# Kernel optimization log

Hardware: AMD Instinct MI355X
Metric: run time of the kernel (lower is better)

## Reference

```python
import jax, jax.numpy as jnp
import numpy as np

D_MODEL = 1024
H = 16           # num_heads
D = 64           # head_dim
HD = H * D       # hd_dim
PHASE_SCALE = 10.0


def _freqs():
    # Multiscale phasor frequencies (H, D): rotary-style per-dim decay,
    # per-head linear scale (reconstruction of generate_multiscale_phasors).
    d = jnp.arange(D, dtype=jnp.float32)
    base = 10000.0 ** (-d / D)                                  # (D,)
    head_scale = (jnp.arange(H, dtype=jnp.float32) + 1.0) / H   # (H,)
    return 2.0 * np.pi * head_scale[:, None] * base[None, :]    # (H, D)


def setup_inputs() -> dict:
    key = jax.random.key(0)
    ks = jax.random.split(key, 4)
    B, T = 2, 8192
    s = 1.0 / np.sqrt(D_MODEL)
    return {
        "x": jax.random.normal(ks[0], (B, T, D_MODEL), jnp.float32),
        "Wk": jax.random.normal(ks[1], (HD, D_MODEL), jnp.float32) * s,
        "Wv": jax.random.normal(ks[2], (HD, D_MODEL), jnp.float32) * s,
        "Wo": jax.random.normal(ks[3], (D_MODEL, HD), jnp.float32) * s,
        "gate": jnp.ones((H, 2), jnp.float32) * 0.5,
    }


def reference(x, Wk, Wv, Wo, gate):
    B, T, C = x.shape
    k_real = (x @ Wk.T).reshape(B, T, H, D)                      # (B,T,H,D)
    v = (x @ Wv.T).reshape(B, T, H, D).astype(jnp.complex64)
    # shared q/k unit-modulus phasors
    k = jnp.exp(1j * (k_real * PHASE_SCALE))                     # complex64
    q = k
    t = jnp.arange(T, dtype=jnp.float32)
    rotors = jnp.exp(1j * (t[:, None, None] * _freqs()[None]))   # (T,H,D)
    scale = jnp.sqrt(jnp.arange(1, T + 1, dtype=jnp.float32))[None, :, None, None]
    # positional path: bind with rotors, accumulate, retrieve with conj rotors
    mem_pos = jnp.cumsum(v * rotors[None], axis=1)
    out_pos = (mem_pos * jnp.conj(rotors)[None]).real / scale
    # associative path: bind with conj of shifted keys, retrieve with q
    k_shifted = jnp.roll(k, shift=1, axis=1).at[:, 0].set(0)
    mem_assoc = jnp.cumsum(v * jnp.conj(k_shifted), axis=1)
    out_assoc = (mem_assoc * q).real / scale
    # gated combine per head
    out = out_pos * gate[None, None, :, 0:1] + out_assoc * gate[None, None, :, 1:2]
    out = out.reshape(B, T, HD)
    return out @ Wo.T
```

## Files before the change

### kernel.cpp

```cpp
#include <hip/hip_runtime.h>
#include <math.h>


#define B_SZ 2
#define T_LEN 8192
#define H_N 16
#define D_N 64
#define HD 1024
#define DM 1024

#define NCH 128
#define CH (T_LEN / NCH)

typedef unsigned short u16;
typedef __attribute__((ext_vector_type(4))) unsigned short u16x4;
typedef __attribute__((ext_vector_type(8))) short s16x8;
typedef __attribute__((ext_vector_type(8))) _Float16 f16x8;
typedef __attribute__((ext_vector_type(4))) float f32x4;

__device__ __forceinline__ u16 f2h(float f) {
    return __builtin_bit_cast(u16, (_Float16)f);
}
__device__ __forceinline__ float h2f(u16 h) {
    return (float)__builtin_bit_cast(_Float16, h);
}

__global__ __launch_bounds__(256) void conv_x_h(
    const float* __restrict__ x, u16* __restrict__ xh)
{
    size_t i = ((size_t)blockIdx.x * 256 + threadIdx.x) * 4;
    float4 v = *reinterpret_cast<const float4*>(&x[i]);
    u16x4 o = { f2h(v.x), f2h(v.y), f2h(v.z), f2h(v.w) };
    *reinterpret_cast<u16x4*>(&xh[i]) = o;
}

__global__ __launch_bounds__(256) void conv_weights(
    const float* __restrict__ Wk, const float* __restrict__ Wv,
    const float* __restrict__ Wo, u16* __restrict__ Wkv, u16* __restrict__ Wob)
{
    size_t i = ((size_t)blockIdx.x * 256 + threadIdx.x) * 4;
    int r = (int)(i >> 10);
    size_t src = i & (1024ull * 1024 - 1);
    float4 v;
    float s = 1.f;
    u16* dst;
    size_t doff;
    if (r < 1024)      { v = *reinterpret_cast<const float4*>(&Wk[src]); s = 10.f; dst = Wkv; doff = i; }
    else if (r < 2048) { v = *reinterpret_cast<const float4*>(&Wv[src]); dst = Wkv; doff = i; }
    else               { v = *reinterpret_cast<const float4*>(&Wo[src]); dst = Wob; doff = src; }
    u16x4 o = { f2h(s * v.x), f2h(s * v.y), f2h(s * v.z), f2h(s * v.w) };
    *reinterpret_cast<u16x4*>(&dst[doff]) = o;
}

#define GBK 64

#define BAR()     asm volatile("s_barrier" ::: "memory")
#define VMCNT4()  asm volatile("s_waitcnt vmcnt(4)" ::: "memory")
#define VMCNT0()  asm volatile("s_waitcnt vmcnt(0)" ::: "memory")
#define LGKM8PRE() asm volatile("s_waitcnt lgkmcnt(8)" ::: "memory")
#define LGKM0_SB() do { asm volatile("s_waitcnt lgkmcnt(0)" ::: "memory"); \
                        __builtin_amdgcn_sched_barrier(0); } while (0)

template <int IMM>
__device__ __forceinline__ s16x8 dsr(unsigned base) {
    s16x8 r;
    asm volatile("ds_read_b128 %0, %1 offset:%2"
                 : "=v"(r) : "v"(base), "n"(IMM));
    return r;
}

__device__ __forceinline__ unsigned lds_addr(const void* p) {
    return (unsigned)(uintptr_t)(const __attribute__((address_space(3))) void*)p;
}

#define MFMA_Q(mh, nh)                                               \
  {                                                                  \
    _Pragma("unroll")                                                \
    for (int ks_ = 0; ks_ < 2; ++ks_)                                \
      _Pragma("unroll")                                              \
      for (int m_ = 0; m_ < 4; ++m_)                                 \
        _Pragma("unroll")                                            \
        for (int n_ = 0; n_ < 2; ++n_)                               \
          acc[(mh)*4 + m_][(nh)*2 + n_] =                            \
            __builtin_amdgcn_mfma_f32_16x16x32_f16(                  \
              __builtin_bit_cast(f16x8, aR[m_][ks_]),                \
              __builtin_bit_cast(f16x8, bR[(nh)*2 + n_][ks_]),       \
              acc[(mh)*4 + m_][(nh)*2 + n_], 0, 0, 0);               \
  }

#define RD_A(ph, ofs)                                                          \
  aR[0][0]=dsr<(ofs)+0>(bA[ph][0]);    aR[1][0]=dsr<(ofs)+2048>(bA[ph][0]);    \
  aR[2][0]=dsr<(ofs)+4096>(bA[ph][0]); aR[3][0]=dsr<(ofs)+6144>(bA[ph][0]);    \
  aR[0][1]=dsr<(ofs)+0>(bA[ph][1]);    aR[1][1]=dsr<(ofs)+2048>(bA[ph][1]);    \
  aR[2][1]=dsr<(ofs)+4096>(bA[ph][1]); aR[3][1]=dsr<(ofs)+6144>(bA[ph][1]);
#define RD_B01(ph)                                                             \
  bR[0][0]=dsr<0>(bB[ph][0]);    bR[1][0]=dsr<2048>(bB[ph][0]);                \
  bR[0][1]=dsr<0>(bB[ph][1]);    bR[1][1]=dsr<2048>(bB[ph][1]);
#define RD_B23(ph)                                                             \
  bR[2][0]=dsr<4096>(bB[ph][0]); bR[3][0]=dsr<6144>(bB[ph][0]);                \
  bR[2][1]=dsr<4096>(bB[ph][1]); bR[3][1]=dsr<6144>(bB[ph][1]);

#define PHASE_GROUP(ph)                                              \
  {                                                                  \
    RD_A(ph, 0); RD_B01(ph); RD_B23(ph);                             \
    LGKM8PRE();                                                      \
    if ((ph) == 0)    { STAGE_A(2*t+1, 1, 0); STAGE_A(2*t+1, 1, 1); }\
    else if (gm)      { STAGE_A(2*t+2, 0, 0); STAGE_A(2*t+2, 0, 1); }\
    BAR(); LGKM0_SB();                                               \
    __builtin_amdgcn_s_setprio(1);                                   \
    MFMA_Q(0, 0); MFMA_Q(0, 1);                                      \
    __builtin_amdgcn_s_setprio(0);                                   \
    BAR();                                                           \
    RD_A(ph, 8192);                                                  \
    if (gm) { STAGE_B(2*t+2+(ph), (ph), 0);                          \
              STAGE_B(2*t+2+(ph), (ph), 1); VMCNT4(); }              \
    else    { VMCNT0(); }                                            \
    BAR(); LGKM0_SB();                                               \
    __builtin_amdgcn_s_setprio(1);                                   \
    MFMA_Q(1, 0); MFMA_Q(1, 1);                                      \
    __builtin_amdgcn_s_setprio(0);                                   \
    BAR();                                                           \
  }

__device__ __forceinline__ void stage_half(
    const u16* __restrict__ g, int ld, int rowbase, int kbase,
    char* ldshalf, int wid, int lane)
{
#pragma unroll
    for (int s = 0; s < 2; ++s) {
        const int slot = s * 512 + wid * 64 + lane;
        const int r = slot >> 3;
        const int cb = ((slot & 7) << 4) ^ ((r & 7) << 4);
        const u16* gp = g + (size_t)(rowbase + r) * ld + kbase + (cb >> 1);
        __builtin_amdgcn_global_load_lds(
            (const __attribute__((address_space(1))) void*)gp,
            (__attribute__((address_space(3))) void*)(ldshalf + s * 8192 + wid * 1024),
            16, 0, 0);
    }
}

__global__ __launch_bounds__(512, 2) void gemm_mfma256(
    const u16* __restrict__ A, int lda, const u16* __restrict__ W, int ldw,
    void* __restrict__ Cv, int ldc, void* __restrict__ Vv, int K, int mode,
    int m_base, int bshift)
{
    __shared__ __align__(16) char lds[131072];

    const int tid  = threadIdx.x;
    const int lane = tid & 63;
    const int wid  = tid >> 6;
    const int wm   = wid >> 2;
    const int wn   = wid & 3;
    const int l15  = lane & 15;
    const int hib  = (lane >> 4) << 4;

    const int flat = blockIdx.y * gridDim.x + blockIdx.x;
    const int xcd  = flat & 7;
    const int c    = flat >> 3;
    const int byl  = c & ((1 << bshift) - 1);
    const int bx   = c >> bshift;
    const int m0   = ((xcd << bshift) + byl) * 256 + m_base;
    const int n0   = bx * 256;

    const int NK2 = K / (2 * GBK);

    f32x4 acc[8][4] = {};
    s16x8 aR[4][2], bR[4][2];

    const int Xl = (l15 & 7) << 4;
    unsigned bA[2][2], bB[2][2];
#pragma unroll
    for (int p2 = 0; p2 < 2; ++p2)
#pragma unroll
        for (int ks = 0; ks < 2; ++ks) {
            bA[p2][ks] = lds_addr(lds) + p2 * 65536 +
                         (wm * 128 + l15) * 128 + ((ks * 64 + hib) ^ Xl);
            bB[p2][ks] = lds_addr(lds) + p2 * 65536 + 32768 +
                         (wn * 64 + l15) * 128 + ((ks * 64 + hib) ^ Xl);
        }

    auto STAGE_A = [&](int kt, int buf, int h) {
        stage_half(A, lda, m0 + h * 128, kt * GBK,
                   (char*)lds + buf * 65536 + h * 16384, wid, lane);
    };
    auto STAGE_B = [&](int kt, int buf, int h) {
        stage_half(W, ldw, n0 + h * 128, kt * GBK,
                   (char*)lds + buf * 65536 + 32768 + h * 16384, wid, lane);
    };

    STAGE_B(0, 0, 0); STAGE_B(0, 0, 1);
    STAGE_A(0, 0, 0); STAGE_A(0, 0, 1);
    STAGE_B(1, 1, 0); STAGE_B(1, 1, 1);
    VMCNT4();
    BAR();

    for (int t = 0; t < NK2; ++t) {
        const bool gm = (t < NK2 - 1);
        PHASE_GROUP(0)
        PHASE_GROUP(1)
    }

    const float TWOPI  = 6.2831853071795864f;
    const float INV2PI = 0.15915494309189535f;
    float* Cf = (float*)Cv;
    u16*   Ph = (u16*)Cv;
    u16*   Vh = (u16*)Vv;
    const bool isPhase = (n0 < 1024);
#pragma unroll
    for (int m = 0; m < 8; ++m) {
#pragma unroll
        for (int n = 0; n < 4; ++n) {
            const int r0  = m0 + wm * 128 + m * 16 + ((lane >> 4) << 2);
            const int col = n0 + wn * 64 + n * 16 + l15;
#pragma unroll
            for (int r = 0; r < 4; ++r) {
                const float val = acc[m][n][r];
                if (mode == 0) {
                    Cf[(size_t)(r0 + r) * ldc + col] = val;
                } else if (isPhase) {
                    float red = fmaf(-TWOPI, rintf(val * INV2PI), val);
                    Ph[(size_t)(r0 + r) * 1024 + col] = f2h(red);
                } else {
                    Vh[(size_t)(r0 + r) * 1024 + (col - 1024)] = f2h(val);
                }
            }
        }
    }
}

__device__ __forceinline__ void rotor_sincos(int t, double fd, float* sr, float* cr)
{
    const double twopi = 6.283185307179586;
    const double inv2pi = 0.15915494309189535;
    double ang = (double)t * fd;
    double n = rint(ang * inv2pi);
    float red = (float)(ang - n * twopi);
    __sincosf(red, sr, cr);
}

__global__ __launch_bounds__(256) void scan_pass1(
    const u16* __restrict__ vArr, const u16* __restrict__ phase,
    float* __restrict__ cs)
{
    int gw = (blockIdx.x * 256 + threadIdx.x) >> 6;
    int d = threadIdx.x & 63;
    int c = gw & (NCH - 1);
    int h = (gw >> 7) & (H_N - 1);
    int b = gw >> 11;

    double fd = 6.283185307179586 * ((double)(h + 1) / 16.0)
              * pow(10000.0, -(double)d / 64.0);

    int t0 = c * CH;
    size_t base = ((size_t)b * T_LEN + t0) * HD + (size_t)h * D_N + d;

    float cr, sr;
    rotor_sincos(t0, fd, &sr, &cr);
    float cf, sf;
    sincosf((float)fd, &sf, &cf);

    float cp = 0.f, spv = 0.f;
    if (t0 > 0) {
        float thp = h2f(phase[base - HD]);
        __sincosf(thp, &spv, &cp);
    }

    float sp_re = 0.f, sp_im = 0.f, sa_re = 0.f, sa_im = 0.f;
    for (int i = 0; i < CH; ++i) {
        size_t idx = base + (size_t)i * HD;
        float v = h2f(vArr[idx]);
        float th = h2f(phase[idx]);
        sp_re = fmaf(v, cr, sp_re);
        sp_im = fmaf(v, sr, sp_im);
        sa_re = fmaf(v, cp, sa_re);
        sa_im = fmaf(-v, spv, sa_im);
        __sincosf(th, &spv, &cp);
        float nc = fmaf(cr, cf, -sr * sf);
        float ns = fmaf(sr, cf,  cr * sf);
        cr = nc; sr = ns;
    }

    const size_t NT = (size_t)B_SZ * H_N * NCH * D_N;
    size_t ci = (size_t)gw * D_N + d;
    cs[ci] = sp_re;
    cs[NT + ci] = sp_im;
    cs[2 * NT + ci] = sa_re;
    cs[3 * NT + ci] = sa_im;
}

__global__ void scan_pass2(float* __restrict__ cs)
{
    int tid = blockIdx.x * blockDim.x + threadIdx.x;
    if (tid >= B_SZ * H_N * D_N) return;
    int d = tid & 63;
    int bh = tid >> 6;
    size_t base = (size_t)bh * NCH * D_N + d;
    const size_t NT = (size_t)B_SZ * H_N * NCH * D_N;
    float r0 = 0.f, r1 = 0.f, r2 = 0.f, r3 = 0.f;
    for (int c = 0; c < NCH; ++c) {
        size_t i = base + (size_t)c * D_N;
        float a = cs[i], b2 = cs[NT + i], c2 = cs[2 * NT + i], d2 = cs[3 * NT + i];
        cs[i] = r0; cs[NT + i] = r1; cs[2 * NT + i] = r2; cs[3 * NT + i] = r3;
        r0 += a; r1 += b2; r2 += c2; r3 += d2;
    }
}

__global__ __launch_bounds__(256) void scan_pass3(
    const u16* __restrict__ vArr, const u16* __restrict__ phase,
    const float* __restrict__ cs, const float* __restrict__ gate,
    u16* __restrict__ y)
{
    int gw = (blockIdx.x * 256 + threadIdx.x) >> 6;
    int d = threadIdx.x & 63;
    int c = gw & (NCH - 1);
    int h = (gw >> 7) & (H_N - 1);
    int b = gw >> 11;

    double fd = 6.283185307179586 * ((double)(h + 1) / 16.0)
              * pow(10000.0, -(double)d / 64.0);
    float g0 = gate[h * 2 + 0];
    float g1 = gate[h * 2 + 1];

    int t0 = c * CH;
    size_t base = ((size_t)b * T_LEN + t0) * HD + (size_t)h * D_N + d;

    const size_t NT = (size_t)B_SZ * H_N * NCH * D_N;
    size_t ci = (size_t)gw * D_N + d;
    float ap_re = cs[ci];
    float ap_im = cs[NT + ci];
    float aa_re = cs[2 * NT + ci];
    float aa_im = cs[3 * NT + ci];

    float cr, sr;
    rotor_sincos(t0, fd, &sr, &cr);
    float cf, sf;
    sincosf((float)fd, &sf, &cf);

    float cp = 0.f, spv = 0.f;
    if (t0 > 0) {
        float thp = h2f(phase[base - HD]);
        __sincosf(thp, &spv, &cp);
    }

    for (int i = 0; i < CH; ++i) {
        int t = t0 + i;
        size_t idx = base + (size_t)i * HD;
        float v = h2f(vArr[idx]);
        float th = h2f(phase[idx]);
        ap_re = fmaf(v, cr, ap_re);
        ap_im = fmaf(v, sr, ap_im);
        aa_re = fmaf(v, cp, aa_re);
        aa_im = fmaf(-v, spv, aa_im);
        float op = fmaf(ap_re, cr, ap_im * sr);
        float ck, sk;
        __sincosf(th, &sk, &ck);
        float oa = fmaf(aa_re, ck, -aa_im * sk);
        float sc = rsqrtf((float)(t + 1));
        y[idx] = f2h((g0 * op + g1 * oa) * sc);
        cp = ck; spv = sk;
        float nc = fmaf(cr, cf, -sr * sf);
        float ns = fmaf(sr, cf,  cr * sf);
        cr = nc; sr = ns;
    }
}

extern "C" void kernel_launch(void* const* d_in, const int* in_sizes, int n_in,
                              void* d_out, int out_size, void* d_ws, size_t ws_size,
                              hipStream_t stream)
{
    const float* x    = (const float*)d_in[0];
    const float* Wk   = (const float*)d_in[1];
    const float* Wv   = (const float*)d_in[2];
    const float* Wo   = (const float*)d_in[3];
    const float* gate = (const float*)d_in[4];
    float* out = (float*)d_out;

    char* wsb = (char*)d_ws;
    u16*   xh   = (u16*)wsb;
    u16*   yb   = (u16*)wsb;
    u16*   vb   = (u16*)(wsb + (32ull << 20));
    float* cs   = (float*)(wsb + (64ull << 20));
    u16*   Wkv  = (u16*)(wsb + (68ull << 20));
    u16*   Wob  = (u16*)(wsb + (72ull << 20));
    u16*   ph16 = (u16*)(wsb + (74ull << 20));

    hipLaunchKernelGGL(conv_x_h, dim3(16384), dim3(256), 0, stream, x, xh);
    hipLaunchKernelGGL(conv_weights, dim3(3072), dim3(256), 0, stream,
                       Wk, Wv, Wo, Wkv, Wob);

    const dim3 gblk(512);

    hipLaunchKernelGGL(gemm_mfma256, dim3(8, 32), gblk, 0, stream,
                       xh, 1024, Wkv, 1024, (void*)ph16, 1024, (void*)vb, 1024, 3,
                       0, 2);
    hipLaunchKernelGGL(gemm_mfma256, dim3(8, 32), gblk, 0, stream,
                       xh, 1024, Wkv, 1024, (void*)ph16, 1024, (void*)vb, 1024, 3,
                       8192, 2);

    const int waves = B_SZ * H_N * NCH;
    hipLaunchKernelGGL(scan_pass1, dim3(waves / 4), dim3(256), 0, stream, vb, ph16, cs);
    hipLaunchKernelGGL(scan_pass2, dim3(8), dim3(256), 0, stream, cs);
    hipLaunchKernelGGL(scan_pass3, dim3(waves / 4), dim3(256), 0, stream, vb, ph16, cs, gate, yb);

    hipLaunchKernelGGL(gemm_mfma256, dim3(4, 64), gblk, 0, stream,
                       yb, 1024, Wob, 1024, (void*)out, HD, (void*)0, 1024, 0,
                       0, 3);
}
```

Before: 183.9 us.

## Chain K and V projections per tile so A stays hot, merge conversion kernels

The two input-conversion kernels become one launch. The two half-M projection GEMMs become a single kernel in which each block first computes its phase tile (the Wk rows) and then its V tile (the Wv rows) for the same rows of x. The phase result is written out mid-loop and the accumulator is reset. This is meant to reuse the same x rows from cache across both products, remove kernel launches, and specialise the GEMMs with compile-time constants in place of runtime mode branches. In exchange, each block now does twice the K-loop work with fewer blocks in the grid, and the block count is reduced to 256, which can hurt load balance.

```diff
diff --git a/kernel.cpp b/kernel.cpp
--- a/kernel.cpp
+++ b/kernel.cpp
@@ -25,31 +25,31 @@
     return (float)__builtin_bit_cast(_Float16, h);
 }
 
-__global__ __launch_bounds__(256) void conv_x_h(
-    const float* __restrict__ x, u16* __restrict__ xh)
+__global__ __launch_bounds__(256) void conv_all(
+    const float* __restrict__ x, const float* __restrict__ Wk,
+    const float* __restrict__ Wv, const float* __restrict__ Wo,
+    u16* __restrict__ xh, u16* __restrict__ Wkv, u16* __restrict__ Wob)
 {
     size_t i = ((size_t)blockIdx.x * 256 + threadIdx.x) * 4;
-    float4 v = *reinterpret_cast<const float4*>(&x[i]);
-    u16x4 o = { f2h(v.x), f2h(v.y), f2h(v.z), f2h(v.w) };
-    *reinterpret_cast<u16x4*>(&xh[i]) = o;
-}
-
-__global__ __launch_bounds__(256) void conv_weights(
-    const float* __restrict__ Wk, const float* __restrict__ Wv,
-    const float* __restrict__ Wo, u16* __restrict__ Wkv, u16* __restrict__ Wob)
-{
-    size_t i = ((size_t)blockIdx.x * 256 + threadIdx.x) * 4;
-    int r = (int)(i >> 10);
-    size_t src = i & (1024ull * 1024 - 1);
-    float4 v;
-    float s = 1.f;
-    u16* dst;
-    size_t doff;
-    if (r < 1024)      { v = *reinterpret_cast<const float4*>(&Wk[src]); s = 10.f; dst = Wkv; doff = i; }
-    else if (r < 2048) { v = *reinterpret_cast<const float4*>(&Wv[src]); dst = Wkv; doff = i; }
-    else               { v = *reinterpret_cast<const float4*>(&Wo[src]); dst = Wob; doff = src; }
-    u16x4 o = { f2h(s * v.x), f2h(s * v.y), f2h(s * v.z), f2h(s * v.w) };
-    *reinterpret_cast<u16x4*>(&dst[doff]) = o;
+    const size_t NX = 16384ull * 1024;
+    if (i < NX) {
+        float4 v = *reinterpret_cast<const float4*>(&x[i]);
+        u16x4 o = { f2h(v.x), f2h(v.y), f2h(v.z), f2h(v.w) };
+        *reinterpret_cast<u16x4*>(&xh[i]) = o;
+    } else {
+        size_t j = i - NX;
+        int r = (int)(j >> 10);
+        size_t src = j & (1024ull * 1024 - 1);
+        float4 v;
+        float s = 1.f;
+        u16* dst;
+        size_t doff;
+        if (r < 1024)      { v = *reinterpret_cast<const float4*>(&Wk[src]); s = 10.f; dst = Wkv; doff = j; }
+        else if (r < 2048) { v = *reinterpret_cast<const float4*>(&Wv[src]); dst = Wkv; doff = j; }
+        else               { v = *reinterpret_cast<const float4*>(&Wo[src]); dst = Wob; doff = src; }
+        u16x4 o = { f2h(s * v.x), f2h(s * v.y), f2h(s * v.z), f2h(s * v.w) };
+        *reinterpret_cast<u16x4*>(&dst[doff]) = o;
+    }
 }
 
 #define GBK 64
@@ -100,28 +100,6 @@
   bR[2][0]=dsr<4096>(bB[ph][0]); bR[3][0]=dsr<6144>(bB[ph][0]);                \
   bR[2][1]=dsr<4096>(bB[ph][1]); bR[3][1]=dsr<6144>(bB[ph][1]);
 
-#define PHASE_GROUP(ph)                                              \
-  {                                                                  \
-    RD_A(ph, 0); RD_B01(ph); RD_B23(ph);                             \
-    LGKM8PRE();                                                      \
-    if ((ph) == 0)    { STAGE_A(2*t+1, 1, 0); STAGE_A(2*t+1, 1, 1); }\
-    else if (gm)      { STAGE_A(2*t+2, 0, 0); STAGE_A(2*t+2, 0, 1); }\
-    BAR(); LGKM0_SB();                                               \
-    __builtin_amdgcn_s_setprio(1);                                   \
-    MFMA_Q(0, 0); MFMA_Q(0, 1);                                      \
-    __builtin_amdgcn_s_setprio(0);                                   \
-    BAR();                                                           \
-    RD_A(ph, 8192);                                                  \
-    if (gm) { STAGE_B(2*t+2+(ph), (ph), 0);                          \
-              STAGE_B(2*t+2+(ph), (ph), 1); VMCNT4(); }              \
-    else    { VMCNT0(); }                                            \
-    BAR(); LGKM0_SB();                                               \
-    __builtin_amdgcn_s_setprio(1);                                   \
-    MFMA_Q(1, 0); MFMA_Q(1, 1);                                      \
-    __builtin_amdgcn_s_setprio(0);                                   \
-    BAR();                                                           \
-  }
-
 __device__ __forceinline__ void stage_half(
     const u16* __restrict__ g, int ld, int rowbase, int kbase,
     char* ldshalf, int wid, int lane)
@@ -139,52 +117,48 @@
     }
 }
 
-__global__ __launch_bounds__(512, 2) void gemm_mfma256(
-    const u16* __restrict__ A, int lda, const u16* __restrict__ W, int ldw,
-    void* __restrict__ Cv, int ldc, void* __restrict__ Vv, int K, int mode,
-    int m_base, int bshift)
+#define GEMM_COMMON_SETUP()                                                    \
+    const int tid  = threadIdx.x;                                              \
+    const int lane = tid & 63;                                                 \
+    const int wid  = tid >> 6;                                                 \
+    const int wm   = wid >> 2;                                                 \
+    const int wn   = wid & 3;                                                  \
+    const int l15  = lane & 15;                                                \
+    const int hib  = (lane >> 4) << 4;                                         \
+    const int flat = blockIdx.y * gridDim.x + blockIdx.x;                      \
+    const int xcd  = flat & 7;                                                 \
+    const int c    = flat >> 3;                                                \
+    const int byl  = c & 7;                                                    \
+    const int bx   = c >> 3;                                                   \
+    const int m0   = (xcd * 8 + byl) * 256;                                    \
+    const int n0   = bx * 256;                                                 \
+    f32x4 acc[8][4] = {};                                                      \
+    s16x8 aR[4][2], bR[4][2];                                                  \
+    const int Xl = (l15 & 7) << 4;                                             \
+    unsigned bA[2][2], bB[2][2];                                               \
+    _Pragma("unroll")                                                          \
+    for (int p2 = 0; p2 < 2; ++p2)                                             \
+        _Pragma("unroll")                                                      \
+        for (int ks = 0; ks < 2; ++ks) {                                       \
+            bA[p2][ks] = lds_addr(lds) + p2 * 65536 +                          \
+                         (wm * 128 + l15) * 128 + ((ks * 64 + hib) ^ Xl);      \
+            bB[p2][ks] = lds_addr(lds) + p2 * 65536 + 32768 +                  \
+                         (wn * 64 + l15) * 128 + ((ks * 64 + hib) ^ Xl);       \
+        }
+
+__global__ __launch_bounds__(512, 2) void gemm_chain(
+    const u16* __restrict__ A, const u16* __restrict__ W,
+    u16* __restrict__ Ph, u16* __restrict__ Vh)
 {
     __shared__ __align__(16) char lds[131072];
-
-    const int tid  = threadIdx.x;
-    const int lane = tid & 63;
-    const int wid  = tid >> 6;
-    const int wm   = wid >> 2;
-    const int wn   = wid & 3;
-    const int l15  = lane & 15;
-    const int hib  = (lane >> 4) << 4;
-
-    const int flat = blockIdx.y * gridDim.x + blockIdx.x;
-    const int xcd  = flat & 7;
-    const int c    = flat >> 3;
-    const int byl  = c & ((1 << bshift) - 1);
-    const int bx   = c >> bshift;
-    const int m0   = ((xcd << bshift) + byl) * 256 + m_base;
-    const int n0   = bx * 256;
-
-    const int NK2 = K / (2 * GBK);
-
-    f32x4 acc[8][4] = {};
-    s16x8 aR[4][2], bR[4][2];
-
-    const int Xl = (l15 & 7) << 4;
-    unsigned bA[2][2], bB[2][2];
-#pragma unroll
-    for (int p2 = 0; p2 < 2; ++p2)
-#pragma unroll
-        for (int ks = 0; ks < 2; ++ks) {
-            bA[p2][ks] = lds_addr(lds) + p2 * 65536 +
-                         (wm * 128 + l15) * 128 + ((ks * 64 + hib) ^ Xl);
-            bB[p2][ks] = lds_addr(lds) + p2 * 65536 + 32768 +
-                         (wn * 64 + l15) * 128 + ((ks * 64 + hib) ^ Xl);
-        }
-
-    auto STAGE_A = [&](int kt, int buf, int h) {
-        stage_half(A, lda, m0 + h * 128, kt * GBK,
+    GEMM_COMMON_SETUP();
+
+    auto STAGE_A = [&](int q, int buf, int h) {
+        stage_half(A, 1024, m0 + h * 128, (q & 15) * GBK,
                    (char*)lds + buf * 65536 + h * 16384, wid, lane);
     };
-    auto STAGE_B = [&](int kt, int buf, int h) {
-        stage_half(W, ldw, n0 + h * 128, kt * GBK,
+    auto STAGE_B = [&](int q, int buf, int h) {
+        stage_half(W, 1024, n0 + ((q >> 4) << 10) + h * 128, (q & 15) * GBK,
                    (char*)lds + buf * 65536 + 32768 + h * 16384, wid, lane);
     };
 
@@ -194,38 +168,140 @@
     VMCNT4();
     BAR();
 
-    for (int t = 0; t < NK2; ++t) {
-        const bool gm = (t < NK2 - 1);
-        PHASE_GROUP(0)
-        PHASE_GROUP(1)
-    }
-
     const float TWOPI  = 6.2831853071795864f;
     const float INV2PI = 0.15915494309189535f;
-    float* Cf = (float*)Cv;
-    u16*   Ph = (u16*)Cv;
-    u16*   Vh = (u16*)Vv;
-    const bool isPhase = (n0 < 1024);
-#pragma unroll
-    for (int m = 0; m < 8; ++m) {
+
+    for (int t = 0; t < 16; ++t) {
+        if (t == 8) {
+#pragma unroll
+            for (int m = 0; m < 8; ++m)
+#pragma unroll
+                for (int n = 0; n < 4; ++n) {
+                    const int r0  = m0 + wm * 128 + m * 16 + ((lane >> 4) << 2);
+                    const int col = n0 + wn * 64 + n * 16 + l15;
+#pragma unroll
+                    for (int r = 0; r < 4; ++r) {
+                        float val = acc[m][n][r];
+                        float red = fmaf(-TWOPI, rintf(val * INV2PI), val);
+                        Ph[(size_t)(r0 + r) * 1024 + col] = f2h(red);
+                        acc[m][n][r] = 0.f;
+                    }
+                }
+        }
+        const bool gm = (t < 15);
+        RD_A(0, 0); RD_B01(0); RD_B23(0);
+        LGKM8PRE();
+        STAGE_A(2 * t + 1, 1, 0); STAGE_A(2 * t + 1, 1, 1);
+        BAR(); LGKM0_SB();
+        __builtin_amdgcn_s_setprio(1);
+        MFMA_Q(0, 0); MFMA_Q(0, 1);
+        __builtin_amdgcn_s_setprio(0);
+        BAR();
+        RD_A(0, 8192);
+        if (gm) { STAGE_B(2 * t + 2, 0, 0); STAGE_B(2 * t + 2, 0, 1); VMCNT4(); }
+        else    { VMCNT0(); }
+        BAR(); LGKM0_SB();
+        __builtin_amdgcn_s_setprio(1);
+        MFMA_Q(1, 0); MFMA_Q(1, 1);
+        __builtin_amdgcn_s_setprio(0);
+        BAR();
+        RD_A(1, 0); RD_B01(1); RD_B23(1);
+        LGKM8PRE();
+        if (gm) { STAGE_A(2 * t + 2, 0, 0); STAGE_A(2 * t + 2, 0, 1); }
+        BAR(); LGKM0_SB();
+        __builtin_amdgcn_s_setprio(1);
+        MFMA_Q(0, 0); MFMA_Q(0, 1);
+        __builtin_amdgcn_s_setprio(0);
+        BAR();
+        RD_A(1, 8192);
+        if (gm) { STAGE_B(2 * t + 3, 1, 0); STAGE_B(2 * t + 3, 1, 1); VMCNT4(); }
+        else    { VMCNT0(); }
+        BAR(); LGKM0_SB();
+        __builtin_amdgcn_s_setprio(1);
+        MFMA_Q(1, 0); MFMA_Q(1, 1);
+        __builtin_amdgcn_s_setprio(0);
+        BAR();
+    }
+
+#pragma unroll
+    for (int m = 0; m < 8; ++m)
 #pragma unroll
         for (int n = 0; n < 4; ++n) {
             const int r0  = m0 + wm * 128 + m * 16 + ((lane >> 4) << 2);
             const int col = n0 + wn * 64 + n * 16 + l15;
 #pragma unroll
-            for (int r = 0; r < 4; ++r) {
-                const float val = acc[m][n][r];
-                if (mode == 0) {
-                    Cf[(size_t)(r0 + r) * ldc + col] = val;
-                } else if (isPhase) {
-                    float red = fmaf(-TWOPI, rintf(val * INV2PI), val);
-                    Ph[(size_t)(r0 + r) * 1024 + col] = f2h(red);
-                } else {
-                    Vh[(size_t)(r0 + r) * 1024 + (col - 1024)] = f2h(val);
-                }
-            }
+            for (int r = 0; r < 4; ++r)
+                Vh[(size_t)(r0 + r) * 1024 + col] = f2h(acc[m][n][r]);
         }
-    }
+}
+
+__global__ __launch_bounds__(512, 2) void gemm_out(
+    const u16* __restrict__ A, const u16* __restrict__ W, float* __restrict__ C)
+{
+    __shared__ __align__(16) char lds[131072];
+    GEMM_COMMON_SETUP();
+
+    auto STAGE_A = [&](int kt, int buf, int h) {
+        stage_half(A, 1024, m0 + h * 128, kt * GBK,
+                   (char*)lds + buf * 65536 + h * 16384, wid, lane);
+    };
+    auto STAGE_B = [&](int kt, int buf, int h) {
+        stage_half(W, 1024, n0 + h * 128, kt * GBK,
+                   (char*)lds + buf * 65536 + 32768 + h * 16384, wid, lane);
+    };
+
+    STAGE_B(0, 0, 0); STAGE_B(0, 0, 1);
+    STAGE_A(0, 0, 0); STAGE_A(0, 0, 1);
+    STAGE_B(1, 1, 0); STAGE_B(1, 1, 1);
+    VMCNT4();
+    BAR();
+
+    for (int t = 0; t < 8; ++t) {
+        const bool gm = (t < 7);
+        RD_A(0, 0); RD_B01(0); RD_B23(0);
+        LGKM8PRE();
+        STAGE_A(2 * t + 1, 1, 0); STAGE_A(2 * t + 1, 1, 1);
+        BAR(); LGKM0_SB();
+        __builtin_amdgcn_s_setprio(1);
+        MFMA_Q(0, 0); MFMA_Q(0, 1);
+        __builtin_amdgcn_s_setprio(0);
+        BAR();
+        RD_A(0, 8192);
+        if (gm) { STAGE_B(2 * t + 2, 0, 0); STAGE_B(2 * t + 2, 0, 1); VMCNT4(); }
+        else    { VMCNT0(); }
+        BAR(); LGKM0_SB();
+        __builtin_amdgcn_s_setprio(1);
+        MFMA_Q(1, 0); MFMA_Q(1, 1);
+        __builtin_amdgcn_s_setprio(0);
+        BAR();
+        RD_A(1, 0); RD_B01(1); RD_B23(1);
+        LGKM8PRE();
+        if (gm) { STAGE_A(2 * t + 2, 0, 0); STAGE_A(2 * t + 2, 0, 1); }
+        BAR(); LGKM0_SB();
+        __builtin_amdgcn_s_setprio(1);
+        MFMA_Q(0, 0); MFMA_Q(0, 1);
+        __builtin_amdgcn_s_setprio(0);
+        BAR();
+        RD_A(1, 8192);
+        if (gm) { STAGE_B(2 * t + 3, 1, 0); STAGE_B(2 * t + 3, 1, 1); VMCNT4(); }
+        else    { VMCNT0(); }
+        BAR(); LGKM0_SB();
+        __builtin_amdgcn_s_setprio(1);
+        MFMA_Q(1, 0); MFMA_Q(1, 1);
+        __builtin_amdgcn_s_setprio(0);
+        BAR();
+    }
+
+#pragma unroll
+    for (int m = 0; m < 8; ++m)
+#pragma unroll
+        for (int n = 0; n < 4; ++n) {
+            const int r0  = m0 + wm * 128 + m * 16 + ((lane >> 4) << 2);
+            const int col = n0 + wn * 64 + n * 16 + l15;
+#pragma unroll
+            for (int r = 0; r < 4; ++r)
+                C[(size_t)(r0 + r) * HD + col] = acc[m][n][r];
+        }
 }
 
 __device__ __forceinline__ void rotor_sincos(int t, double fd, float* sr, float* cr)
@@ -384,25 +460,18 @@
     u16*   Wob  = (u16*)(wsb + (72ull << 20));
     u16*   ph16 = (u16*)(wsb + (74ull << 20));
 
-    hipLaunchKernelGGL(conv_x_h, dim3(16384), dim3(256), 0, stream, x, xh);
-    hipLaunchKernelGGL(conv_weights, dim3(3072), dim3(256), 0, stream,
-                       Wk, Wv, Wo, Wkv, Wob);
+    hipLaunchKernelGGL(conv_all, dim3(19456), dim3(256), 0, stream,
+                       x, Wk, Wv, Wo, xh, Wkv, Wob);
 
     const dim3 gblk(512);
 
-    hipLaunchKernelGGL(gemm_mfma256, dim3(8, 32), gblk, 0, stream,
-                       xh, 1024, Wkv, 1024, (void*)ph16, 1024, (void*)vb, 1024, 3,
-                       0, 2);
-    hipLaunchKernelGGL(gemm_mfma256, dim3(8, 32), gblk, 0, stream,
-                       xh, 1024, Wkv, 1024, (void*)ph16, 1024, (void*)vb, 1024, 3,
-                       8192, 2);
+    hipLaunchKernelGGL(gemm_chain, dim3(4, 64), gblk, 0, stream,
+                       xh, Wkv, ph16, vb);
 
     const int waves = B_SZ * H_N * NCH;
     hipLaunchKernelGGL(scan_pass1, dim3(waves / 4), dim3(256), 0, stream, vb, ph16, cs);
     hipLaunchKernelGGL(scan_pass2, dim3(8), dim3(256), 0, stream, cs);
     hipLaunchKernelGGL(scan_pass3, dim3(waves / 4), dim3(256), 0, stream, vb, ph16, cs, gate, yb);
 
-    hipLaunchKernelGGL(gemm_mfma256, dim3(4, 64), gblk, 0, stream,
-                       yb, 1024, Wob, 1024, (void*)out, HD, (void*)0, 1024, 0,
-                       0, 3);
-}
+    hipLaunchKernelGGL(gemm_out, dim3(4, 64), gblk, 0, stream, yb, Wob, out);
+}
```

Result: slower. 260.1 us (+41.5%).
